# Kernel optimization log

Hardware: AMD Instinct MI355X
Metric: run time of the kernel (lower is better)

Reference implementation:

```python
import jax, jax.numpy as jnp
import numpy as np
from jax import lax

ALPHA = 0.5
EPS = 1e-5  # BatchNorm eps (training-mode batch stats, faithful to nn.BatchNorm2d default)


def _conv1x1(x, w, b):
    # w: [O, C, 1, 1]
    return jnp.einsum('bchw,oc->bohw', x, w[:, :, 0, 0]) + b[None, :, None, None]


def _conv3x3(x, w, b):
    y = lax.conv_general_dilated(x, w, (1, 1), ((1, 1), (1, 1)),
                                 dimension_numbers=('NCHW', 'OIHW', 'NCHW'))
    return y + b[None, :, None, None]


def _convT3x3(x, w, b):
    # PyTorch ConvTranspose2d weight layout: [in, out, kh, kw]
    y = lax.conv_transpose(x, w, (1, 1), ((1, 1), (1, 1)),
                           dimension_numbers=('NCHW', 'IOHW', 'NCHW'),
                           transpose_kernel=True)
    return y + b[None, :, None, None]


def _lin(z, w, b):
    # z: [B, N, C], w: [C, C] (PyTorch Linear layout: out, in)
    return jnp.einsum('bnc,oc->bno', z, w) + b


def setup_inputs() -> dict:
    key = jax.random.key(0)
    ks = jax.random.split(key, 32)
    B, C, H, W = 8, 256, 56, 56
    R = C // 16  # reduction=16

    def n(k, shape, s=0.05):
        return jax.random.normal(k, shape, jnp.float32) * s

    return {
        'x': jax.random.normal(ks[0], (B, C, H, W), jnp.float32),
        'hard_neg': jax.random.normal(ks[1], (B, C, H, W), jnp.float32),
        'attr_c1_w': n(ks[2], (R, C, 1, 1)), 'attr_c1_b': n(ks[3], (R,)),
        'attr_c2_w': n(ks[4], (C, R, 1, 1)), 'attr_c2_b': n(ks[5], (C,)),
        'adj_w': n(ks[6], (C, 2 * C, 1, 1)), 'adj_b': n(ks[7], (C,)),
        'tex_c1_w': n(ks[8], (C, C, 3, 3)), 'tex_c1_b': n(ks[9], (C,)),
        'tex_c2_w': n(ks[10], (C, C, 3, 3)), 'tex_c2_b': n(ks[11], (C,)),
        'q_attr_w': n(ks[12], (C, C)), 'q_attr_b': n(ks[13], (C,)),
        'k_attr_w': n(ks[14], (C, C)), 'k_attr_b': n(ks[15], (C,)),
        'v_attr_w': n(ks[16], (C, C)), 'v_attr_b': n(ks[17], (C,)),
        'q_tex_w': n(ks[18], (C, C)), 'q_tex_b': n(ks[19], (C,)),
        'k_tex_w': n(ks[20], (C, C)), 'k_tex_b': n(ks[21], (C,)),
        'v_tex_w': n(ks[22], (C, C)), 'v_tex_b': n(ks[23], (C,)),
        'out_w': n(ks[24], (C, C, 1, 1)), 'out_b': n(ks[25], (C,)),
        'bn_g': jnp.ones((C,), jnp.float32), 'bn_b': jnp.zeros((C,), jnp.float32),
    }


def reference(x, hard_neg, attr_c1_w, attr_c1_b, attr_c2_w, attr_c2_b, adj_w, adj_b,
              tex_c1_w, tex_c1_b, tex_c2_w, tex_c2_b,
              q_attr_w, q_attr_b, k_attr_w, k_attr_b, v_attr_w, v_attr_b,
              q_tex_w, q_tex_b, k_tex_w, k_tex_b, v_tex_w, v_tex_b,
              out_w, out_b, bn_g, bn_b):
    b, c, h, w = x.shape
    # attribute branch (squeeze-excite-like 1x1 convs + concat + 1x1 adjust)
    a = jax.nn.relu(_conv1x1(x, attr_c1_w, attr_c1_b))
    a = jax.nn.relu(_conv1x1(a, attr_c2_w, attr_c2_b))
    a = _conv1x1(jnp.concatenate([a, x], axis=1), adj_w, adj_b)
    # texture branch (3x3 conv + relu + 3x3 conv-transpose), modulated by attr
    t = jax.nn.relu(_conv3x3(hard_neg, tex_c1_w, tex_c1_b))
    t = _convT3x3(t, tex_c2_w, tex_c2_b)
    t = t * a
    # flatten spatial tokens: [B, N, C], N = h*w
    af = a.reshape(b, c, h * w).transpose(0, 2, 1)
    tf = t.reshape(b, c, h * w).transpose(0, 2, 1)
    scale = 1.0 / jnp.sqrt(jnp.asarray(c, jnp.float32))
    Qa, Ka, Va = _lin(af, q_attr_w, q_attr_b), _lin(af, k_attr_w, k_attr_b), _lin(af, v_attr_w, v_attr_b)
    Qt, Kt, Vt = _lin(tf, q_tex_w, q_tex_b), _lin(tf, k_tex_w, k_tex_b), _lin(tf, v_tex_w, v_tex_b)
    # full NxN single-head attention (faithful to the hand-rolled softmax(QK^T)V)
    Aa = jax.nn.softmax(jnp.einsum('bnd,bmd->bnm', Qa, Ka) * scale, axis=-1)
    oa = jnp.einsum('bnm,bmd->bnd', Aa, Va)
    At = jax.nn.softmax(jnp.einsum('bnd,bmd->bnm', Qt, Kt) * scale, axis=-1)
    ot = jnp.einsum('bnm,bmd->bnd', At, Vt)
    o = ALPHA * oa + (1.0 - ALPHA) * ot
    o = o.transpose(0, 2, 1).reshape(b, c, h, w)
    o = _conv1x1(o, out_w, out_b) + x
    # BatchNorm2d in training mode: biased batch stats over (B, H, W)
    mean = jnp.mean(o, axis=(0, 2, 3), keepdims=True)
    var = jnp.var(o, axis=(0, 2, 3), keepdims=True)
    o = (o - mean) / jnp.sqrt(var + EPS)
    return o * bn_g[None, :, None, None] + bn_b[None, :, None, None]
```

## Files before the change

### kernel.cpp

```cpp
#include <hip/hip_runtime.h>
#include <hip/hip_fp16.h>

#define BB 8
#define C 256
#define HH 56
#define WW 56
#define NN 3136
#define RR 16
#define NT (NN/16)
#define PW 58

typedef _Float16 half8 __attribute__((ext_vector_type(8)));
typedef _Float16 half4v __attribute__((ext_vector_type(4)));
typedef float floatx4 __attribute__((ext_vector_type(4)));

#define AS1 __attribute__((address_space(1)))
#define AS3 __attribute__((address_space(3)))

__device__ __forceinline__ void gload16(const _Float16* gsrc, _Float16* ldst) {
  __builtin_amdgcn_global_load_lds((const AS1 unsigned int*)(const void*)gsrc,
                                   (AS3 unsigned int*)(void*)ldst, 16, 0, 0);
}

__global__ __launch_bounds__(256) void attr_kernel(
    const float* __restrict__ x,
    const float* __restrict__ w1T, const float* __restrict__ b1,
    const float* __restrict__ w2, const float* __restrict__ b2,
    const float* __restrict__ wadjT, const float* __restrict__ badj,
    float* __restrict__ a_out)
{
  __shared__ float xs[C][20];
  __shared__ float a2s[C][20];
  __shared__ float a1s[RR][20];
  const int tile = blockIdx.x;
  const int b = tile / NT;
  const int p0 = (tile % NT) * 16;
  const int t = threadIdx.x;

  {
    const float* xb = x + ((size_t)b * C + t) * NN + p0;
    const float4* xb4 = (const float4*)xb;
    float* row = xs[t];
#pragma unroll
    for (int g = 0; g < 4; ++g) {
      float4 v = xb4[g];
      row[g * 4 + 0] = v.x; row[g * 4 + 1] = v.y;
      row[g * 4 + 2] = v.z; row[g * 4 + 3] = v.w;
    }
  }
  __syncthreads();

  {
    const int r = t & 15, pp = t >> 4;
    float acc = b1[r];
    for (int c = 0; c < C; ++c) acc += w1T[c * 16 + r] * xs[c][pp];
    a1s[r][pp] = fmaxf(acc, 0.f);
  }
  __syncthreads();

  {
    const int o = t;
    float acc[16];
    const float bias = b2[o];
#pragma unroll
    for (int p = 0; p < 16; ++p) acc[p] = bias;
    const float* wr = w2 + o * RR;
    for (int k = 0; k < RR; ++k) {
      const float w = wr[k];
#pragma unroll
      for (int p = 0; p < 16; ++p) acc[p] += w * a1s[k][p];
    }
    float* row = a2s[o];
#pragma unroll
    for (int p = 0; p < 16; ++p) row[p] = fmaxf(acc[p], 0.f);
  }
  __syncthreads();

  {
    const int o = t;
    float acc[16];
    const float bias = badj[o];
#pragma unroll
    for (int p = 0; p < 16; ++p) acc[p] = bias;
    const float* wTa = wadjT + o;
    for (int k = 0; k < C; ++k) {
      const float w = wTa[k * C];
      const float4* ar = (const float4*)a2s[k];
#pragma unroll
      for (int g = 0; g < 4; ++g) {
        float4 v = ar[g];
        acc[g * 4 + 0] += w * v.x; acc[g * 4 + 1] += w * v.y;
        acc[g * 4 + 2] += w * v.z; acc[g * 4 + 3] += w * v.w;
      }
    }
    const float* wTx = wadjT + C * C + o;
    for (int k = 0; k < C; ++k) {
      const float w = wTx[k * C];
      const float4* xr = (const float4*)xs[k];
#pragma unroll
      for (int g = 0; g < 4; ++g) {
        float4 v = xr[g];
        acc[g * 4 + 0] += w * v.x; acc[g * 4 + 1] += w * v.y;
        acc[g * 4 + 2] += w * v.z; acc[g * 4 + 3] += w * v.w;
      }
    }
    float* op = a_out + ((size_t)b * C + o) * NN + p0;
    float4* op4 = (float4*)op;
#pragma unroll
    for (int g = 0; g < 4; ++g)
      op4[g] = make_float4(acc[g * 4 + 0], acc[g * 4 + 1], acc[g * 4 + 2], acc[g * 4 + 3]);
  }
}

__global__ __launch_bounds__(256) void wprep_attr_kernel(
    const float* __restrict__ w1, const float* __restrict__ wadj,
    float* __restrict__ w1T, float* __restrict__ wadjT)
{
  const int i = blockIdx.x * 256 + threadIdx.x;
  if (i < RR * C) {
    const int c = i >> 4, r = i & 15;
    w1T[i] = w1[r * C + c];
  } else {
    const int j = i - RR * C;
    const int k = j >> 8, o = j & 255;
    wadjT[j] = wadj[(size_t)o * (2 * C) + k];
  }
}

__global__ __launch_bounds__(256) void wprep_kernel(
    const float* __restrict__ tw1, const float* __restrict__ tw2,
    _Float16* __restrict__ w1h, _Float16* __restrict__ w2h)
{
  const int i = blockIdx.x * 256 + threadIdx.x;
  const int tap = i >> 16;
  const int rem = i & 65535;
  const int o = rem >> 8;
  const int c = rem & 255;
  w1h[i] = (_Float16)tw1[((size_t)o * C + c) * 9 + tap];
  w2h[i] = (_Float16)tw2[((size_t)o * C + c) * 9 + (8 - tap)];
}

__global__ __launch_bounds__(256) void wprep_qkv_kernel(
    const float* __restrict__ m0, const float* __restrict__ m1,
    const float* __restrict__ m2, const float* __restrict__ m3,
    const float* __restrict__ m4, const float* __restrict__ m5,
    const float* __restrict__ m6, _Float16* __restrict__ Whall)
{
  const int i = blockIdx.x * 256 + threadIdx.x;
  const int mat = i >> 16, rem = i & 65535;
  const float* s;
  switch (mat) {
    case 0: s = m0; break; case 1: s = m1; break; case 2: s = m2; break;
    case 3: s = m3; break; case 4: s = m4; break; case 5: s = m5; break;
    default: s = m6; break;
  }
  Whall[i] = (_Float16)s[rem];
}

__global__ __launch_bounds__(256) void padzero_kernel(
    _Float16* __restrict__ buf1, _Float16* __restrict__ buf2)
{
  const int bid = blockIdx.x;
  _Float16* buf = (bid < BB * PW) ? buf1 : buf2;
  const int rb = bid % (BB * PW);
  const int b = rb / PW, r = rb % PW;
  _Float16* row = buf + ((size_t)b * PW + r) * PW * C;
  const float4 z = make_float4(0.f, 0.f, 0.f, 0.f);
  if (r == 0 || r == PW - 1) {
    for (int i = threadIdx.x; i < PW * C / 8; i += 256) ((float4*)row)[i] = z;
  } else {
    const int i = threadIdx.x;
    if (i < 32) ((float4*)row)[i] = z;
    else if (i < 64) ((float4*)(row + (PW - 1) * C))[i - 32] = z;
  }
}

__global__ __launch_bounds__(256) void hnprep_kernel(
    const float* __restrict__ hn, _Float16* __restrict__ hnpad)
{
  __shared__ float xs[C][17];
  const int tile = blockIdx.x;
  const int b = tile / NT;
  const int p0 = (tile % NT) * 16;
  const int t = threadIdx.x;
  {
    const float4* sb = (const float4*)(hn + ((size_t)b * C + t) * NN + p0);
    float* row = xs[t];
#pragma unroll
    for (int g = 0; g < 4; ++g) {
      float4 v = sb[g];
      row[g * 4 + 0] = v.x; row[g * 4 + 1] = v.y;
      row[g * 4 + 2] = v.z; row[g * 4 + 3] = v.w;
    }
  }
  __syncthreads();
  const int p = t >> 4, c0 = (t & 15) * 16;
  const int pg = p0 + p;
  const int h = pg / WW, w = pg % WW;
  __align__(16) _Float16 tmp[16];
#pragma unroll
  for (int j = 0; j < 16; ++j) tmp[j] = (_Float16)xs[c0 + j][p];
  _Float16* dst = hnpad + (((size_t)b * PW + h + 1) * PW + w + 1) * C + c0;
  ((uint4*)dst)[0] = ((uint4*)tmp)[0];
  ((uint4*)dst)[1] = ((uint4*)tmp)[1];
}

__global__ __launch_bounds__(512, 1) void conv_mfma_kernel(
    const _Float16* __restrict__ inpad, const _Float16* __restrict__ wh,
    const float* __restrict__ bias, const float* __restrict__ amul,
    _Float16* __restrict__ out_h, float* __restrict__ out_f, int mode)
{
  __shared__ _Float16 Is[4 * 58 * 256];

  const int bid = blockIdx.x;
  const int b = bid & 7;
  const int h0 = (bid >> 3) * 2;
  const int t = threadIdx.x;
  const int w = t >> 6;
  const int lane = t & 63;
  const int col = lane & 15, quad = lane >> 4;
  const int q16 = quad * 16;

  const _Float16* inb = inpad + (size_t)b * PW * PW * C;

  {
    const _Float16* strip = inb + (size_t)h0 * PW * C;
    for (int i = w; i < 116; i += 8) {
      const int cb = i * 64;
      const int chunk = cb + lane;
      const int pp = chunk >> 5, cc = chunk & 31;
      gload16(strip + ((size_t)pp * 32 + (cc ^ (pp & 7))) * 8,
              Is + (size_t)cb * 8);
    }
  }
  asm volatile("s_waitcnt vmcnt(0)" ::: "memory");
  __syncthreads();

  int ppb[7];
#pragma unroll
  for (int nt = 0; nt < 7; ++nt) {
    const int opx = nt * 16 + col;
    const int ro = (opx >= 56) ? 1 : 0;
    ppb[nt] = ro * 58 + (opx - ro * 56);
  }

  floatx4 acc[2][7];
#pragma unroll
  for (int mt = 0; mt < 2; ++mt)
#pragma unroll
    for (int nt = 0; nt < 7; ++nt) acc[mt][nt] = (floatx4){0.f, 0.f, 0.f, 0.f};

  for (int tap = 0; tap < 9; ++tap) {
    const int dy = tap / 3, dx = tap - dy * 3;
    const int pd = dy * 58 + dx;
    int bb[7], xx[7];
#pragma unroll
    for (int nt = 0; nt < 7; ++nt) {
      const int pp = ppb[nt] + pd;
      bb[nt] = pp * 512;
      xx[nt] = (pp & 7) << 4;
    }
    const _Float16* wr0 = wh + (size_t)tap * C * C +
                          (size_t)(w * 32 + col) * C + quad * 8;
#pragma unroll
    for (int kc = 0; kc < 8; ++kc) {
      const half8 A0 = *(const half8*)(wr0 + kc * 32);
      const half8 A1 = *(const half8*)(wr0 + 16 * C + kc * 32);
#pragma unroll
      for (int nt = 0; nt < 7; ++nt) {
        const half8 Bv = *(const half8*)((const char*)Is + bb[nt] +
                                         ((kc * 64 + q16) ^ xx[nt]));
        acc[0][nt] = __builtin_amdgcn_mfma_f32_16x16x32_f16(A0, Bv, acc[0][nt], 0, 0, 0);
        acc[1][nt] = __builtin_amdgcn_mfma_f32_16x16x32_f16(A1, Bv, acc[1][nt], 0, 0, 0);
      }
    }
  }

#pragma unroll
  for (int mt = 0; mt < 2; ++mt) {
    const int o = w * 32 + mt * 16 + quad * 4;
    const float* bp = bias + o;
    const float b0 = bp[0], b1_ = bp[1], b2_ = bp[2], b3_ = bp[3];
    if (mode == 0) {
#pragma unroll
      for (int nt = 0; nt < 7; ++nt) {
        const int opx = nt * 16 + col;
        const int ro = (opx >= 56) ? 1 : 0;
        const int wpx = opx - ro * 56;
        __align__(8) _Float16 hv[4];
        hv[0] = (_Float16)fmaxf(acc[mt][nt][0] + b0, 0.f);
        hv[1] = (_Float16)fmaxf(acc[mt][nt][1] + b1_, 0.f);
        hv[2] = (_Float16)fmaxf(acc[mt][nt][2] + b2_, 0.f);
        hv[3] = (_Float16)fmaxf(acc[mt][nt][3] + b3_, 0.f);
        _Float16* dst = out_h +
            (((size_t)b * PW + h0 + ro + 1) * PW + wpx + 1) * C + o;
        *(uint2*)dst = *(uint2*)hv;
      }
    } else {
      const float bbv[4] = {b0, b1_, b2_, b3_};
#pragma unroll
      for (int nt = 0; nt < 7; ++nt) {
        const int opx = nt * 16 + col;
        const int ro = (opx >= 56) ? 1 : 0;
        const int wpx = opx - ro * 56;
        const int p = (h0 + ro) * WW + wpx;
#pragma unroll
        for (int r = 0; r < 4; ++r) {
          const size_t idx = ((size_t)(b * C + o + r)) * NN + p;
          out_f[idx] = (acc[mt][nt][r] + bbv[r]) * amul[idx];
        }
      }
    }
  }
}

__device__ inline half8 ld_frag(const _Float16* p) {
  union { half8 h8; half4v h4[2]; } u;
  u.h4[0] = *(const half4v*)p;
  u.h4[1] = *(const half4v*)(p + 4);
  return u.h8;
}

__global__ __launch_bounds__(256) void qkv_mfma_kernel(
    const float* __restrict__ src, const _Float16* __restrict__ Wh,
    const float* __restrict__ bq, const float* __restrict__ bk,
    const float* __restrict__ bv,
    __half* __restrict__ Q, __half* __restrict__ K, __half* __restrict__ Vt)
{
  __shared__ _Float16 Ss[32][264];
  const int bid = blockIdx.x;
  const int b = bid & 7;
  const int p0 = (bid >> 3) * 32;
  const int t = threadIdx.x;
  const int w = t >> 6, lane = t & 63;
  const int col = lane & 15, quad = lane >> 4;

  {
    const float4* sp = (const float4*)(src + ((size_t)b * C + t) * NN + p0);
    float v[32];
#pragma unroll
    for (int g = 0; g < 8; ++g) {
      const float4 f = sp[g];
      v[g * 4 + 0] = f.x; v[g * 4 + 1] = f.y;
      v[g * 4 + 2] = f.z; v[g * 4 + 3] = f.w;
    }
#pragma unroll
    for (int px = 0; px < 32; ++px) Ss[px][t] = (_Float16)v[px];
  }
  __syncthreads();

  floatx4 acc[12][2];
#pragma unroll
  for (int i = 0; i < 12; ++i)
#pragma unroll
    for (int nt = 0; nt < 2; ++nt) acc[i][nt] = (floatx4){0.f, 0.f, 0.f, 0.f};

  for (int k0 = 0; k0 < 256; k0 += 32) {
    half8 bf[2];
    bf[0] = ld_frag(&Ss[col][k0 + quad * 8]);
    bf[1] = ld_frag(&Ss[16 + col][k0 + quad * 8]);
#pragma unroll
    for (int i = 0; i < 12; ++i) {
      const int mtg = w * 12 + i;
      const half8 af = *(const half8*)(Wh + (size_t)mtg * 4096 + col * 256 + k0 + quad * 8);
      acc[i][0] = __builtin_amdgcn_mfma_f32_16x16x32_f16(af, bf[0], acc[i][0], 0, 0, 0);
      acc[i][1] = __builtin_amdgcn_mfma_f32_16x16x32_f16(af, bf[1], acc[i][1], 0, 0, 0);
    }
  }

#pragma unroll
  for (int i = 0; i < 12; ++i) {
    const int mtg = w * 12 + i;
    const int s = mtg >> 4;
    const int crow = (mtg & 15) * 16 + quad * 4;
    const float* bp = (s == 0 ? bq : (s == 1 ? bk : bv)) + crow;
    const float4 b4 = *(const float4*)bp;
    const float bb[4] = {b4.x, b4.y, b4.z, b4.w};
#pragma unroll
    for (int nt = 0; nt < 2; ++nt) {
      const int px = p0 + nt * 16 + col;
      if (s == 2) {
#pragma unroll
        for (int r = 0; r < 4; ++r)
          Vt[((size_t)(b * C) + crow + r) * NN + px] =
              __float2half((acc[i][nt][r] + bb[r]) * 0.5f);
      } else if (s == 0) {
        __half* dst = Q + ((size_t)(b * NN) + px) * C + crow;
        __align__(8) __half hv[4];
#pragma unroll
        for (int r = 0; r < 4; ++r)
          hv[r] = __float2half((acc[i][nt][r] + bb[r]) * 0.0625f);
        *(uint2*)dst = *(uint2*)hv;
      } else {
        __half* dst = K + ((size_t)(b * NN) + px) * C + crow;
        __align__(8) __half hv[4];
#pragma unroll
        for (int r = 0; r < 4; ++r) hv[r] = __float2half(acc[i][nt][r] + bb[r]);
        *(uint2*)dst = *(uint2*)hv;
      }
    }
  }
}

__global__ __launch_bounds__(448, 2) void flash11_kernel(
    const __half* __restrict__ Qg, const __half* __restrict__ Kg,
    const __half* __restrict__ Vtg, __half* __restrict__ O16, int accumulate)
{
  __shared__ _Float16 Ks[2][64 * 256];
  __shared__ _Float16 Vs[2][256 * 64];
  __shared__ _Float16 Pb[7][16][76];

  const int bid = blockIdx.x;
  const int b = bid & 7;
  const int q0 = (bid >> 3) * 112;
  const int t = threadIdx.x;
  const int w = t >> 6;
  const int lane = t & 63;
  const int col = lane & 15;
  const int quad = lane >> 4;

  const _Float16* Kb = (const _Float16*)Kg + (size_t)(b * NN) * C;
  const _Float16* Vb = (const _Float16*)Vtg + (size_t)(b * C) * NN;

  const _Float16* Qp = (const _Float16*)Qg +
      ((size_t)(b * NN) + q0 + w * 16 + col) * C + quad * 8;
  half8 Qf[8];
#pragma unroll
  for (int s = 0; s < 8; ++s) Qf[s] = *(const half8*)(Qp + s * 32);

  floatx4 Ov[16];
#pragma unroll
  for (int n = 0; n < 16; ++n) Ov[n] = (floatx4){0.f, 0.f, 0.f, 0.f};
  float m[4] = {-1e30f, -1e30f, -1e30f, -1e30f};
  float lp[4] = {0.f, 0.f, 0.f, 0.f};

  auto stage = [&](int buf, int key0) {
#pragma unroll
    for (int i = 0; i < 5; ++i) {
      const int cb = i * 448 + w * 64;
      if (cb < 2048) {
        const int c = cb + lane;
        const int krow = c >> 5, kcir = c & 31;
        gload16(Kb + (size_t)(key0 + krow) * C + ((kcir ^ (krow & 7)) * 8),
                &Ks[buf][(size_t)cb * 8]);
      }
    }
#pragma unroll
    for (int i = 0; i < 5; ++i) {
      const int cb = i * 448 + w * 64;
      if (cb < 2048) {
        const int c = cb + lane;
        const int vch = c >> 3, vcir = c & 7;
        gload16(Vb + (size_t)vch * NN + key0 + ((vcir ^ (vch & 7)) * 8),
                &Vs[buf][(size_t)cb * 8]);
      }
    }
  };

  stage(0, 0);
  asm volatile("s_waitcnt vmcnt(0)" ::: "memory");
  __syncthreads();

  for (int kb = 0; kb < 49; ++kb) {
    const int cur = kb & 1;
    if (kb + 1 < 49) stage(cur ^ 1, (kb + 1) * 64);

    const _Float16* Kc = Ks[cur];
    const _Float16* Vc = Vs[cur];

    floatx4 Sv[4];
    __builtin_amdgcn_s_setprio(1);
#pragma unroll
    for (int nt = 0; nt < 4; ++nt) {
      floatx4 acc = (floatx4){0.f, 0.f, 0.f, 0.f};
      const int krow = nt * 16 + col;
      const char* kbase = (const char*)Kc + krow * 512;
      const int kx = (krow & 7) << 4;
#pragma unroll
      for (int s = 0; s < 8; ++s) {
        const half8 bf = *(const half8*)(kbase + ((s * 64 + quad * 16) ^ kx));
        acc = __builtin_amdgcn_mfma_f32_16x16x32_f16(Qf[s], bf, acc, 0, 0, 0);
      }
      Sv[nt] = acc;
    }
    __builtin_amdgcn_s_setprio(0);

    float f[4];
    bool grow = false;
#pragma unroll
    for (int r = 0; r < 4; ++r) {
      float v = fmaxf(fmaxf(Sv[0][r], Sv[1][r]), fmaxf(Sv[2][r], Sv[3][r]));
      v = fmaxf(v, __shfl_xor(v, 1));
      v = fmaxf(v, __shfl_xor(v, 2));
      v = fmaxf(v, __shfl_xor(v, 4));
      v = fmaxf(v, __shfl_xor(v, 8));
      const float mn = fmaxf(m[r], v);
      f[r] = __expf(m[r] - mn);
      grow = grow || (v > m[r]);
      m[r] = mn;
    }
#pragma unroll
    for (int r = 0; r < 4; ++r) {
      float rs = 0.f;
#pragma unroll
      for (int nt = 0; nt < 4; ++nt) {
        const float p = __expf(Sv[nt][r] - m[r]);
        Sv[nt][r] = p;
        rs += p;
      }
      lp[r] = lp[r] * f[r] + rs;
    }

#pragma unroll
    for (int nt = 0; nt < 4; ++nt)
#pragma unroll
      for (int r = 0; r < 4; ++r)
        Pb[w][quad * 4 + r][nt * 16 + col] = (_Float16)Sv[nt][r];

    if (__any(grow)) {
      const floatx4 fv = {f[0], f[1], f[2], f[3]};
#pragma unroll
      for (int n = 0; n < 16; ++n) Ov[n] *= fv;
    }

    const half8 pa0 = ld_frag(&Pb[w][col][quad * 8]);
    const half8 pa1 = ld_frag(&Pb[w][col][32 + quad * 8]);

    __builtin_amdgcn_s_setprio(1);
#pragma unroll
    for (int nt2 = 0; nt2 < 16; ++nt2) {
      const int vrow = nt2 * 16 + col;
      const char* vbase = (const char*)Vc + vrow * 128;
      const int vx = (vrow & 7) << 4;
      const half8 bv0 = *(const half8*)(vbase + ((quad * 16) ^ vx));
      const half8 bv1 = *(const half8*)(vbase + ((64 + quad * 16) ^ vx));
      Ov[nt2] = __builtin_amdgcn_mfma_f32_16x16x32_f16(pa0, bv0, Ov[nt2], 0, 0, 0);
      Ov[nt2] = __builtin_amdgcn_mfma_f32_16x16x32_f16(pa1, bv1, Ov[nt2], 0, 0, 0);
    }
    __builtin_amdgcn_s_setprio(0);

    asm volatile("s_waitcnt vmcnt(0)" ::: "memory");
    __syncthreads();
  }

  float inv[4];
#pragma unroll
  for (int r = 0; r < 4; ++r) {
    float s = lp[r];
    s += __shfl_xor(s, 1);
    s += __shfl_xor(s, 2);
    s += __shfl_xor(s, 4);
    s += __shfl_xor(s, 8);
    inv[r] = 1.f / s;
  }
#pragma unroll
  for (int nt2 = 0; nt2 < 16; ++nt2) {
#pragma unroll
    for (int r = 0; r < 4; ++r) {
      const float val = Ov[nt2][r] * inv[r];
      __half* dst = O16 + ((size_t)(b * NN) + q0 + w * 16 + quad * 4 + r) * C +
                    nt2 * 16 + col;
      if (accumulate) *dst = __float2half(val + __half2float(*dst));
      else *dst = __float2half(val);
    }
  }
}

__global__ __launch_bounds__(256) void outconv_mfma_kernel(
    const __half* __restrict__ O16, const _Float16* __restrict__ owh,
    const float* __restrict__ ob, const float* __restrict__ x,
    float* __restrict__ o)
{
  const int bid = blockIdx.x;
  const int b = bid & 7;
  const int p0 = (bid >> 3) * 64;
  const int t = threadIdx.x;
  const int w = t >> 6, lane = t & 63;
  const int col = lane & 15, quad = lane >> 4;

  floatx4 acc[4][4];
#pragma unroll
  for (int mt = 0; mt < 4; ++mt)
#pragma unroll
    for (int nt = 0; nt < 4; ++nt) acc[mt][nt] = (floatx4){0.f, 0.f, 0.f, 0.f};

  const _Float16* Ob = (const _Float16*)O16 + (size_t)(b * NN) * C;

  for (int k0 = 0; k0 < 256; k0 += 32) {
    half8 bf[4];
#pragma unroll
    for (int nt = 0; nt < 4; ++nt)
      bf[nt] = *(const half8*)(Ob + (size_t)(p0 + nt * 16 + col) * C + k0 + quad * 8);
#pragma unroll
    for (int mt = 0; mt < 4; ++mt) {
      const int crow = w * 64 + mt * 16 + col;
      const half8 af = *(const half8*)(owh + (size_t)crow * 256 + k0 + quad * 8);
#pragma unroll
      for (int nt = 0; nt < 4; ++nt)
        acc[mt][nt] = __builtin_amdgcn_mfma_f32_16x16x32_f16(af, bf[nt], acc[mt][nt], 0, 0, 0);
    }
  }

#pragma unroll
  for (int mt = 0; mt < 4; ++mt) {
    const int c0 = w * 64 + mt * 16 + quad * 4;
    const float4 b4 = *(const float4*)(ob + c0);
    const float bb[4] = {b4.x, b4.y, b4.z, b4.w};
#pragma unroll
    for (int nt = 0; nt < 4; ++nt) {
      const int px = p0 + nt * 16 + col;
#pragma unroll
      for (int r = 0; r < 4; ++r) {
        const size_t idx = ((size_t)(b * C) + c0 + r) * NN + px;
        o[idx] = acc[mt][nt][r] + bb[r] + x[idx];
      }
    }
  }
}

__global__ __launch_bounds__(256) void stats_kernel(
    const float* __restrict__ o, float* __restrict__ stats)
{
  const int c = blockIdx.x, t = threadIdx.x;
  float s = 0.f, sq = 0.f;
  for (int b = 0; b < BB; ++b) {
    const float* p = o + ((size_t)b * C + c) * NN;
    for (int idx = t; idx < NN; idx += 256) {
      const float v = p[idx];
      s += v; sq += v * v;
    }
  }
#pragma unroll
  for (int off = 32; off >= 1; off >>= 1) {
    s += __shfl_xor(s, off);
    sq += __shfl_xor(sq, off);
  }
  __shared__ float red[8];
  const int wv = t >> 6;
  if ((t & 63) == 0) { red[wv] = s; red[4 + wv] = sq; }
  __syncthreads();
  if (t == 0) {
    s = red[0] + red[1] + red[2] + red[3];
    sq = red[4] + red[5] + red[6] + red[7];
    stats[c] = s;
    stats[C + c] = sq;
  }
}

__global__ __launch_bounds__(256) void bn_kernel(
    const float* __restrict__ o, const float* __restrict__ stats,
    const float* __restrict__ g, const float* __restrict__ bta,
    float* __restrict__ out)
{
  const size_t idx = (size_t)blockIdx.x * 256 + threadIdx.x;
  const float inv_n = 1.f / (float)(BB * NN);
  float4 v = ((const float4*)o)[idx];
  const int c = (int)((idx * 4 / NN) % C);
  const float mean = stats[c] * inv_n;
  const float var = stats[C + c] * inv_n - mean * mean;
  const float sc = rsqrtf(var + 1e-5f) * g[c];
  const float sh = bta[c] - mean * sc;
  v.x = v.x * sc + sh; v.y = v.y * sc + sh;
  v.z = v.z * sc + sh; v.w = v.w * sc + sh;
  ((float4*)out)[idx] = v;
}

extern "C" void kernel_launch(void* const* d_in, const int* in_sizes, int n_in,
                              void* d_out, int out_size, void* d_ws, size_t ws_size,
                              hipStream_t stream)
{
  const float* x    = (const float*)d_in[0];
  const float* hn   = (const float*)d_in[1];
  const float* w1   = (const float*)d_in[2];  const float* b1   = (const float*)d_in[3];
  const float* w2   = (const float*)d_in[4];  const float* b2   = (const float*)d_in[5];
  const float* wadj = (const float*)d_in[6];  const float* badj = (const float*)d_in[7];
  const float* tw1  = (const float*)d_in[8];  const float* tb1  = (const float*)d_in[9];
  const float* tw2  = (const float*)d_in[10]; const float* tb2  = (const float*)d_in[11];
  const float* qaw  = (const float*)d_in[12]; const float* qab  = (const float*)d_in[13];
  const float* kaw  = (const float*)d_in[14]; const float* kab  = (const float*)d_in[15];
  const float* vaw  = (const float*)d_in[16]; const float* vab  = (const float*)d_in[17];
  const float* qtw  = (const float*)d_in[18]; const float* qtb  = (const float*)d_in[19];
  const float* ktw  = (const float*)d_in[20]; const float* ktb  = (const float*)d_in[21];
  const float* vtw  = (const float*)d_in[22]; const float* vtb  = (const float*)d_in[23];
  const float* ow   = (const float*)d_in[24]; const float* obias= (const float*)d_in[25];
  const float* bng  = (const float*)d_in[26]; const float* bnb  = (const float*)d_in[27];

  char* ws = (char*)d_ws;
  const size_t TENS  = (size_t)BB * C * NN * sizeof(float);
  const size_t HTENS = (size_t)BB * NN * C * sizeof(__half);
  const size_t PADT  = (size_t)BB * PW * PW * C * sizeof(_Float16)
                       + 16384;
  const size_t WT    = (size_t)9 * C * C * sizeof(_Float16);
  float*    a     = (float*)(ws);
  float*    tt    = (float*)(ws + TENS);
  _Float16* hnpad = (_Float16*)(ws + 2 * TENS);
  _Float16* t1pad = (_Float16*)(ws + 2 * TENS + PADT);
  _Float16* w1h   = (_Float16*)(ws + 2 * TENS + 2 * PADT);
  _Float16* w2h   = (_Float16*)(ws + 2 * TENS + 2 * PADT + WT);
  __half*   Q     = (__half*)(ws + 2 * TENS);
  __half*   K     = (__half*)(ws + 2 * TENS + HTENS);
  __half*   Vt    = (__half*)(ws + 2 * TENS + 2 * HTENS);
  float*    stats = (float*)(ws + 2 * TENS + 3 * HTENS);
  _Float16* Whall = (_Float16*)(ws + 2 * TENS + 3 * HTENS + 4096);
  float*    w1T   = (float*)(ws + 2 * TENS + 3 * HTENS + 4096 + 7 * 65536 * 2);
  float*    wadjT = w1T + RR * C;
  __half*   O16   = (__half*)a;

  const int PIX_TILES = BB * NT;
  const int CONV_BLKS = BB * 28;
  const int FLASH_BLKS = BB * 28;
  const int QKV_BLKS = BB * (NN / 32);
  const int OUT_BLKS = BB * (NN / 64);

  wprep_kernel<<<9 * C * C / 256, 256, 0, stream>>>(tw1, tw2, w1h, w2h);
  wprep_qkv_kernel<<<7 * C * C / 256, 256, 0, stream>>>(
      qaw, kaw, vaw, qtw, ktw, vtw, ow, Whall);
  wprep_attr_kernel<<<(RR * C + 2 * C * C) / 256, 256, 0, stream>>>(
      w1, wadj, w1T, wadjT);
  padzero_kernel<<<2 * BB * PW, 256, 0, stream>>>(hnpad, t1pad);
  hnprep_kernel<<<PIX_TILES, 256, 0, stream>>>(hn, hnpad);
  attr_kernel<<<PIX_TILES, 256, 0, stream>>>(x, w1T, b1, w2, b2, wadjT, badj, a);
  conv_mfma_kernel<<<CONV_BLKS, 512, 0, stream>>>(hnpad, w1h, tb1, nullptr, t1pad, nullptr, 0);
  conv_mfma_kernel<<<CONV_BLKS, 512, 0, stream>>>(t1pad, w2h, tb2, a, nullptr, tt, 1);

  qkv_mfma_kernel<<<QKV_BLKS, 256, 0, stream>>>(a, Whall, qab, kab, vab, Q, K, Vt);
  flash11_kernel<<<FLASH_BLKS, 448, 0, stream>>>(Q, K, Vt, O16, 0);
  qkv_mfma_kernel<<<QKV_BLKS, 256, 0, stream>>>(tt, Whall + 3 * 65536, qtb, ktb, vtb, Q, K, Vt);
  flash11_kernel<<<FLASH_BLKS, 448, 0, stream>>>(Q, K, Vt, O16, 1);

  float* o = tt;
  outconv_mfma_kernel<<<OUT_BLKS, 256, 0, stream>>>(O16, Whall + 6 * 65536, obias, x, o);
  stats_kernel<<<C, 256, 0, stream>>>(o, stats);
  bn_kernel<<<(BB * C * NN / 4) / 256, 256, 0, stream>>>(o, stats, bng, bnb, (float*)d_out);
}
```

Measured before the change: 923.7 us.

## Merge both attention branches into one flash launch with 32-row warp tiles

The two flash-attention launches are combined into one kernel whose blocks pick the attr or tex branch from the block index. Each warp now handles 32 query rows instead of 16, so every K/V tile staged in shared memory is reused across twice as many MFMA rows. The accumulate-into-O read-modify-write is replaced by two separate outputs that the output conv sums on load. The cost is more accumulator registers per thread, a new workspace layout with aliased buffers, and a single wave of 224 blocks.

```diff
diff --git a/kernel.cpp b/kernel.cpp
--- a/kernel.cpp
+++ b/kernel.cpp
@@ -402,37 +402,52 @@
   }
 }
 
-__global__ __launch_bounds__(448, 2) void flash11_kernel(
-    const __half* __restrict__ Qg, const __half* __restrict__ Kg,
-    const __half* __restrict__ Vtg, __half* __restrict__ O16, int accumulate)
+__global__ __launch_bounds__(448, 2) void flash12_kernel(
+    const __half* __restrict__ Q0g, const __half* __restrict__ K0g,
+    const __half* __restrict__ V0g,
+    const __half* __restrict__ Q1g, const __half* __restrict__ K1g,
+    const __half* __restrict__ V1g,
+    __half* __restrict__ O0, __half* __restrict__ O1)
 {
   __shared__ _Float16 Ks[2][64 * 256];
   __shared__ _Float16 Vs[2][256 * 64];
-  __shared__ _Float16 Pb[7][16][76];
+  __shared__ _Float16 Pb[7][32][68];
 
   const int bid = blockIdx.x;
-  const int b = bid & 7;
-  const int q0 = (bid >> 3) * 112;
+  const int vb = bid & 15;
+  const int b = vb & 7;
+  const int br = vb >> 3;
+  const int q0 = (bid >> 4) * 224;
   const int t = threadIdx.x;
   const int w = t >> 6;
   const int lane = t & 63;
   const int col = lane & 15;
   const int quad = lane >> 4;
 
-  const _Float16* Kb = (const _Float16*)Kg + (size_t)(b * NN) * C;
-  const _Float16* Vb = (const _Float16*)Vtg + (size_t)(b * C) * NN;
-
-  const _Float16* Qp = (const _Float16*)Qg +
-      ((size_t)(b * NN) + q0 + w * 16 + col) * C + quad * 8;
-  half8 Qf[8];
-#pragma unroll
-  for (int s = 0; s < 8; ++s) Qf[s] = *(const half8*)(Qp + s * 32);
-
-  floatx4 Ov[16];
-#pragma unroll
-  for (int n = 0; n < 16; ++n) Ov[n] = (floatx4){0.f, 0.f, 0.f, 0.f};
-  float m[4] = {-1e30f, -1e30f, -1e30f, -1e30f};
-  float lp[4] = {0.f, 0.f, 0.f, 0.f};
+  const _Float16* Qg = (const _Float16*)(br ? Q1g : Q0g);
+  const _Float16* Kb = (const _Float16*)(br ? K1g : K0g) + (size_t)(b * NN) * C;
+  const _Float16* Vb = (const _Float16*)(br ? V1g : V0g) + (size_t)(b * C) * NN;
+  __half* Og = br ? O1 : O0;
+
+  half8 Qf[2][8];
+#pragma unroll
+  for (int mt = 0; mt < 2; ++mt) {
+    const _Float16* Qp = Qg +
+        ((size_t)(b * NN) + q0 + w * 32 + mt * 16 + col) * C + quad * 8;
+#pragma unroll
+    for (int s = 0; s < 8; ++s) Qf[mt][s] = *(const half8*)(Qp + s * 32);
+  }
+
+  floatx4 Ov[2][16];
+#pragma unroll
+  for (int mt = 0; mt < 2; ++mt)
+#pragma unroll
+    for (int n = 0; n < 16; ++n) Ov[mt][n] = (floatx4){0.f, 0.f, 0.f, 0.f};
+  float m[2][4], lp[2][4];
+#pragma unroll
+  for (int mt = 0; mt < 2; ++mt)
+#pragma unroll
+    for (int r = 0; r < 4; ++r) { m[mt][r] = -1e30f; lp[mt][r] = 0.f; }
 
   auto stage = [&](int buf, int key0) {
 #pragma unroll
@@ -468,63 +483,74 @@
     const _Float16* Kc = Ks[cur];
     const _Float16* Vc = Vs[cur];
 
-    floatx4 Sv[4];
+    floatx4 Sv[2][4];
     __builtin_amdgcn_s_setprio(1);
 #pragma unroll
     for (int nt = 0; nt < 4; ++nt) {
-      floatx4 acc = (floatx4){0.f, 0.f, 0.f, 0.f};
       const int krow = nt * 16 + col;
       const char* kbase = (const char*)Kc + krow * 512;
       const int kx = (krow & 7) << 4;
+      floatx4 a0 = (floatx4){0.f, 0.f, 0.f, 0.f};
+      floatx4 a1 = (floatx4){0.f, 0.f, 0.f, 0.f};
 #pragma unroll
       for (int s = 0; s < 8; ++s) {
         const half8 bf = *(const half8*)(kbase + ((s * 64 + quad * 16) ^ kx));
-        acc = __builtin_amdgcn_mfma_f32_16x16x32_f16(Qf[s], bf, acc, 0, 0, 0);
-      }
-      Sv[nt] = acc;
+        a0 = __builtin_amdgcn_mfma_f32_16x16x32_f16(Qf[0][s], bf, a0, 0, 0, 0);
+        a1 = __builtin_amdgcn_mfma_f32_16x16x32_f16(Qf[1][s], bf, a1, 0, 0, 0);
+      }
+      Sv[0][nt] = a0;
+      Sv[1][nt] = a1;
     }
     __builtin_amdgcn_s_setprio(0);
 
-    float f[4];
-    bool grow = false;
-#pragma unroll
-    for (int r = 0; r < 4; ++r) {
-      float v = fmaxf(fmaxf(Sv[0][r], Sv[1][r]), fmaxf(Sv[2][r], Sv[3][r]));
-      v = fmaxf(v, __shfl_xor(v, 1));
-      v = fmaxf(v, __shfl_xor(v, 2));
-      v = fmaxf(v, __shfl_xor(v, 4));
-      v = fmaxf(v, __shfl_xor(v, 8));
-      const float mn = fmaxf(m[r], v);
-      f[r] = __expf(m[r] - mn);
-      grow = grow || (v > m[r]);
-      m[r] = mn;
-    }
-#pragma unroll
-    for (int r = 0; r < 4; ++r) {
-      float rs = 0.f;
-#pragma unroll
-      for (int nt = 0; nt < 4; ++nt) {
-        const float p = __expf(Sv[nt][r] - m[r]);
-        Sv[nt][r] = p;
-        rs += p;
-      }
-      lp[r] = lp[r] * f[r] + rs;
-    }
-
-#pragma unroll
-    for (int nt = 0; nt < 4; ++nt)
-#pragma unroll
-      for (int r = 0; r < 4; ++r)
-        Pb[w][quad * 4 + r][nt * 16 + col] = (_Float16)Sv[nt][r];
-
-    if (__any(grow)) {
-      const floatx4 fv = {f[0], f[1], f[2], f[3]};
-#pragma unroll
-      for (int n = 0; n < 16; ++n) Ov[n] *= fv;
-    }
-
-    const half8 pa0 = ld_frag(&Pb[w][col][quad * 8]);
-    const half8 pa1 = ld_frag(&Pb[w][col][32 + quad * 8]);
+#pragma unroll
+    for (int mt = 0; mt < 2; ++mt) {
+      float f[4];
+      bool grow = false;
+#pragma unroll
+      for (int r = 0; r < 4; ++r) {
+        float v = fmaxf(fmaxf(Sv[mt][0][r], Sv[mt][1][r]),
+                        fmaxf(Sv[mt][2][r], Sv[mt][3][r]));
+        v = fmaxf(v, __shfl_xor(v, 1));
+        v = fmaxf(v, __shfl_xor(v, 2));
+        v = fmaxf(v, __shfl_xor(v, 4));
+        v = fmaxf(v, __shfl_xor(v, 8));
+        const float mn = fmaxf(m[mt][r], v);
+        f[r] = __expf(m[mt][r] - mn);
+        grow = grow || (v > m[mt][r]);
+        m[mt][r] = mn;
+      }
+#pragma unroll
+      for (int r = 0; r < 4; ++r) {
+        float rs = 0.f;
+#pragma unroll
+        for (int nt = 0; nt < 4; ++nt) {
+          const float p = __expf(Sv[mt][nt][r] - m[mt][r]);
+          Sv[mt][nt][r] = p;
+          rs += p;
+        }
+        lp[mt][r] = lp[mt][r] * f[r] + rs;
+      }
+
+#pragma unroll
+      for (int nt = 0; nt < 4; ++nt)
+#pragma unroll
+        for (int r = 0; r < 4; ++r)
+          Pb[w][mt * 16 + quad * 4 + r][nt * 16 + col] = (_Float16)Sv[mt][nt][r];
+
+      if (__any(grow)) {
+        const floatx4 fv = {f[0], f[1], f[2], f[3]};
+#pragma unroll
+        for (int n = 0; n < 16; ++n) Ov[mt][n] *= fv;
+      }
+    }
+
+    half8 pa[2][2];
+#pragma unroll
+    for (int mt = 0; mt < 2; ++mt) {
+      pa[mt][0] = ld_frag(&Pb[w][mt * 16 + col][quad * 8]);
+      pa[mt][1] = ld_frag(&Pb[w][mt * 16 + col][32 + quad * 8]);
+    }
 
     __builtin_amdgcn_s_setprio(1);
 #pragma unroll
@@ -534,8 +560,10 @@
       const int vx = (vrow & 7) << 4;
       const half8 bv0 = *(const half8*)(vbase + ((quad * 16) ^ vx));
       const half8 bv1 = *(const half8*)(vbase + ((64 + quad * 16) ^ vx));
-      Ov[nt2] = __builtin_amdgcn_mfma_f32_16x16x32_f16(pa0, bv0, Ov[nt2], 0, 0, 0);
-      Ov[nt2] = __builtin_amdgcn_mfma_f32_16x16x32_f16(pa1, bv1, Ov[nt2], 0, 0, 0);
+      Ov[0][nt2] = __builtin_amdgcn_mfma_f32_16x16x32_f16(pa[0][0], bv0, Ov[0][nt2], 0, 0, 0);
+      Ov[0][nt2] = __builtin_amdgcn_mfma_f32_16x16x32_f16(pa[0][1], bv1, Ov[0][nt2], 0, 0, 0);
+      Ov[1][nt2] = __builtin_amdgcn_mfma_f32_16x16x32_f16(pa[1][0], bv0, Ov[1][nt2], 0, 0, 0);
+      Ov[1][nt2] = __builtin_amdgcn_mfma_f32_16x16x32_f16(pa[1][1], bv1, Ov[1][nt2], 0, 0, 0);
     }
     __builtin_amdgcn_s_setprio(0);
 
@@ -543,31 +571,34 @@
     __syncthreads();
   }
 
-  float inv[4];
-#pragma unroll
-  for (int r = 0; r < 4; ++r) {
-    float s = lp[r];
-    s += __shfl_xor(s, 1);
-    s += __shfl_xor(s, 2);
-    s += __shfl_xor(s, 4);
-    s += __shfl_xor(s, 8);
-    inv[r] = 1.f / s;
-  }
-#pragma unroll
-  for (int nt2 = 0; nt2 < 16; ++nt2) {
+#pragma unroll
+  for (int mt = 0; mt < 2; ++mt) {
+    float inv[4];
 #pragma unroll
     for (int r = 0; r < 4; ++r) {
-      const float val = Ov[nt2][r] * inv[r];
-      __half* dst = O16 + ((size_t)(b * NN) + q0 + w * 16 + quad * 4 + r) * C +
-                    nt2 * 16 + col;
-      if (accumulate) *dst = __float2half(val + __half2float(*dst));
-      else *dst = __float2half(val);
+      float s = lp[mt][r];
+      s += __shfl_xor(s, 1);
+      s += __shfl_xor(s, 2);
+      s += __shfl_xor(s, 4);
+      s += __shfl_xor(s, 8);
+      inv[r] = 1.f / s;
+    }
+#pragma unroll
+    for (int nt2 = 0; nt2 < 16; ++nt2) {
+#pragma unroll
+      for (int r = 0; r < 4; ++r) {
+        const float val = Ov[mt][nt2][r] * inv[r];
+        __half* dst = Og + ((size_t)(b * NN) + q0 + w * 32 + mt * 16 +
+                            quad * 4 + r) * C + nt2 * 16 + col;
+        *dst = __float2half(val);
+      }
     }
   }
 }
 
 __global__ __launch_bounds__(256) void outconv_mfma_kernel(
-    const __half* __restrict__ O16, const _Float16* __restrict__ owh,
+    const __half* __restrict__ O16a, const __half* __restrict__ O16b,
+    const _Float16* __restrict__ owh,
     const float* __restrict__ ob, const float* __restrict__ x,
     float* __restrict__ o)
 {
@@ -584,13 +615,18 @@
 #pragma unroll
     for (int nt = 0; nt < 4; ++nt) acc[mt][nt] = (floatx4){0.f, 0.f, 0.f, 0.f};
 
-  const _Float16* Ob = (const _Float16*)O16 + (size_t)(b * NN) * C;
+  const _Float16* Oa = (const _Float16*)O16a + (size_t)(b * NN) * C;
+  const _Float16* Obf = (const _Float16*)O16b + (size_t)(b * NN) * C;
 
   for (int k0 = 0; k0 < 256; k0 += 32) {
     half8 bf[4];
 #pragma unroll
-    for (int nt = 0; nt < 4; ++nt)
-      bf[nt] = *(const half8*)(Ob + (size_t)(p0 + nt * 16 + col) * C + k0 + quad * 8);
+    for (int nt = 0; nt < 4; ++nt) {
+      const size_t off = (size_t)(p0 + nt * 16 + col) * C + k0 + quad * 8;
+      const half8 va = *(const half8*)(Oa + off);
+      const half8 vb = *(const half8*)(Obf + off);
+      bf[nt] = va + vb;
+    }
 #pragma unroll
     for (int mt = 0; mt < 4; ++mt) {
       const int crow = w * 64 + mt * 16 + col;
@@ -690,25 +726,32 @@
   const size_t HTENS = (size_t)BB * NN * C * sizeof(__half);
   const size_t PADT  = (size_t)BB * PW * PW * C * sizeof(_Float16)
                        + 16384;
-  const size_t WT    = (size_t)9 * C * C * sizeof(_Float16);
   float*    a     = (float*)(ws);
   float*    tt    = (float*)(ws + TENS);
   _Float16* hnpad = (_Float16*)(ws + 2 * TENS);
   _Float16* t1pad = (_Float16*)(ws + 2 * TENS + PADT);
+  const size_t WT = (size_t)9 * C * C * sizeof(_Float16);
   _Float16* w1h   = (_Float16*)(ws + 2 * TENS + 2 * PADT);
   _Float16* w2h   = (_Float16*)(ws + 2 * TENS + 2 * PADT + WT);
-  __half*   Q     = (__half*)(ws + 2 * TENS);
-  __half*   K     = (__half*)(ws + 2 * TENS + HTENS);
-  __half*   Vt    = (__half*)(ws + 2 * TENS + 2 * HTENS);
+  __half*   Q1    = (__half*)(ws + 2 * TENS);
+  __half*   K1    = (__half*)(ws + 2 * TENS + HTENS);
+  __half*   Vt1   = (__half*)(ws + 2 * TENS + 2 * HTENS);
   float*    stats = (float*)(ws + 2 * TENS + 3 * HTENS);
   _Float16* Whall = (_Float16*)(ws + 2 * TENS + 3 * HTENS + 4096);
   float*    w1T   = (float*)(ws + 2 * TENS + 3 * HTENS + 4096 + 7 * 65536 * 2);
   float*    wadjT = w1T + RR * C;
-  __half*   O16   = (__half*)a;
+  const size_t TAIL0 = 2 * TENS + 3 * HTENS + 4096 + 7 * 65536 * 2 +
+                       (size_t)RR * C * 4 + (size_t)2 * C * C * 4;
+  __half*   Q2    = (__half*)(ws);
+  __half*   K2    = (__half*)(ws + HTENS);
+  __half*   Vt2   = (__half*)(ws + TAIL0);
+  __half*   O16a  = (__half*)(ws + TENS);
+  __half*   O16b  = (__half*)(ws + TENS + HTENS);
+  float*    o     = (float*)(ws + 2 * TENS);
 
   const int PIX_TILES = BB * NT;
   const int CONV_BLKS = BB * 28;
-  const int FLASH_BLKS = BB * 28;
+  const int FLASH_BLKS = 224;
   const int QKV_BLKS = BB * (NN / 32);
   const int OUT_BLKS = BB * (NN / 64);
 
@@ -723,13 +766,12 @@
   conv_mfma_kernel<<<CONV_BLKS, 512, 0, stream>>>(hnpad, w1h, tb1, nullptr, t1pad, nullptr, 0);
   conv_mfma_kernel<<<CONV_BLKS, 512, 0, stream>>>(t1pad, w2h, tb2, a, nullptr, tt, 1);
 
-  qkv_mfma_kernel<<<QKV_BLKS, 256, 0, stream>>>(a, Whall, qab, kab, vab, Q, K, Vt);
-  flash11_kernel<<<FLASH_BLKS, 448, 0, stream>>>(Q, K, Vt, O16, 0);
-  qkv_mfma_kernel<<<QKV_BLKS, 256, 0, stream>>>(tt, Whall + 3 * 65536, qtb, ktb, vtb, Q, K, Vt);
-  flash11_kernel<<<FLASH_BLKS, 448, 0, stream>>>(Q, K, Vt, O16, 1);
-
-  float* o = tt;
-  outconv_mfma_kernel<<<OUT_BLKS, 256, 0, stream>>>(O16, Whall + 6 * 65536, obias, x, o);
+  qkv_mfma_kernel<<<QKV_BLKS, 256, 0, stream>>>(a, Whall, qab, kab, vab, Q1, K1, Vt1);
+  qkv_mfma_kernel<<<QKV_BLKS, 256, 0, stream>>>(tt, Whall + 3 * 65536, qtb, ktb, vtb, Q2, K2, Vt2);
+  flash12_kernel<<<FLASH_BLKS, 448, 0, stream>>>(Q1, K1, Vt1, Q2, K2, Vt2, O16a, O16b);
+
+  outconv_mfma_kernel<<<OUT_BLKS, 256, 0, stream>>>(
+      O16a, O16b, Whall + 6 * 65536, obias, x, o);
   stats_kernel<<<C, 256, 0, stream>>>(o, stats);
   bn_kernel<<<(BB * C * NN / 4) / 256, 256, 0, stream>>>(o, stats, bng, bnb, (float*)d_out);
 }
```

After: 1.169 ms. 26.6% more time.
